# Optimization experiments

Hardware: AMD Instinct MI355X
Metric: run time of the kernel (lower is better)

## Reference

```python
import jax, jax.numpy as jnp
import numpy as np

NUM_HEADS = 32


def setup_inputs() -> dict:
    key = jax.random.key(0)
    ks = jax.random.split(key, 6)
    B, S, E = 1, 2048, 2560
    return {
        "hidden_states": jax.random.normal(ks[0], (B, S, E), dtype=jnp.float32),
        "attention_mask": jnp.zeros((B, 1, 1, S), dtype=jnp.float32),
        "position_bias": jax.random.normal(ks[1], (NUM_HEADS, S, S), dtype=jnp.float32),
        "c_attn_w": jax.random.normal(ks[2], (E, 3 * E), dtype=jnp.float32) * 0.02,
        "c_attn_b": jax.random.normal(ks[3], (3 * E,), dtype=jnp.float32) * 0.02,
        "c_proj_w": jax.random.normal(ks[4], (E, E), dtype=jnp.float32) * 0.02,
        "c_proj_b": jax.random.normal(ks[5], (E,), dtype=jnp.float32) * 0.02,
    }


def reference(hidden_states, attention_mask, position_bias, c_attn_w, c_attn_b, c_proj_w, c_proj_b):
    B, S, E = hidden_states.shape
    H = NUM_HEADS
    D = E // H  # head_dim = 80

    # Fused QKV projection (GPT2-style Conv1D: x @ W + b)
    qkv = hidden_states @ c_attn_w + c_attn_b            # [B, S, 3E]
    q, k, v = jnp.split(qkv, 3, axis=-1)

    def split_heads(t):
        return t.reshape(B, S, H, D).transpose(0, 2, 1, 3)  # [B, H, S, D]

    q, k, v = split_heads(q), split_heads(k), split_heads(v)

    # muP scaling: attn_scale_power=1.0 -> divide by head_dim (not sqrt)
    scores = jnp.einsum("bhqd,bhkd->bhqk", q, k) / jnp.asarray(D, q.dtype)
    scores = scores + attention_mask                     # additive mask [B,1,1,S]
    scores = scores + position_bias[None]                # ALiBi bias [1,H,S,S]

    attn = jax.nn.softmax(scores, axis=-1)               # dropout p=0 -> identity
    out = jnp.einsum("bhqk,bhkd->bhqd", attn, v)         # [B, H, S, D]
    out = out.transpose(0, 2, 1, 3).reshape(B, S, E)     # merge heads

    out = out @ c_proj_w + c_proj_b                      # output projection
    return out
```

## Files before the change

kernel.cpp:

```cpp
#include <hip/hip_runtime.h>
#include <stdint.h>

#define S_LEN 2048
#define EMB   2560
#define NH    32
#define HD    80
#define DP    96

typedef __bf16 bf16x8 __attribute__((ext_vector_type(8)));
typedef float  f32x4  __attribute__((ext_vector_type(4)));

__device__ __forceinline__ ushort f2bf(float x) {
    union { float f; uint32_t u; } v; v.f = x;
    return (ushort)((v.u + 0x7FFFu + ((v.u >> 16) & 1u)) >> 16);
}

__device__ __forceinline__ bf16x8 ldg8(const ushort* p) {
    return *reinterpret_cast<const bf16x8*>(p);
}

__device__ __forceinline__ void gload_lds16(const void* g, void* l) {
    __builtin_amdgcn_global_load_lds((__attribute__((address_space(1))) void*)g,
                                     (__attribute__((address_space(3))) void*)l,
                                     16, 0, 0);
}

__global__ void cvt_f32_bf16(const float* __restrict__ in, ushort* __restrict__ out, int n4) {
    int i = blockIdx.x * blockDim.x + threadIdx.x;
    if (i >= n4) return;
    float4 v = reinterpret_cast<const float4*>(in)[i];
    ushort4 r;
    r.x = f2bf(v.x); r.y = f2bf(v.y); r.z = f2bf(v.z); r.w = f2bf(v.w);
    reinterpret_cast<ushort4*>(out)[i] = r;
}

__global__ void transpose_cvt(const float* __restrict__ in, ushort* __restrict__ out, int R, int C) {
    __shared__ float tile[32][33];
    const int bx = blockIdx.x << 5;
    const int by = blockIdx.y << 5;
    const int tx = threadIdx.x, ty = threadIdx.y;
#pragma unroll
    for (int i = 0; i < 4; ++i)
        tile[ty + 8 * i][tx] = in[(size_t)(by + ty + 8 * i) * C + bx + tx];
    __syncthreads();
#pragma unroll
    for (int i = 0; i < 4; ++i)
        out[(size_t)(bx + ty + 8 * i) * R + by + tx] = f2bf(tile[tx][ty + 8 * i]);
}

__global__ void transpose_v(const ushort* __restrict__ V, ushort* __restrict__ VT) {
    __shared__ ushort tile[32][33];
    const int h  = blockIdx.z;
    const int bx = blockIdx.x << 5;
    const int by = blockIdx.y << 5;
    const int tx = threadIdx.x, ty = threadIdx.y;
    const ushort* vin  = V  + (size_t)h * S_LEN * HD;
    ushort*       vout = VT + (size_t)h * HD * S_LEN;
#pragma unroll
    for (int i = 0; i < 4; ++i) {
        int d = bx + tx, s = by + ty + 8 * i;
        tile[ty + 8 * i][tx] = (d < HD) ? vin[(size_t)s * HD + d] : (ushort)0;
    }
    __syncthreads();
#pragma unroll
    for (int i = 0; i < 4; ++i) {
        int d = bx + ty + 8 * i, s = by + tx;
        if (d < HD) vout[(size_t)d * S_LEN + s] = tile[tx][ty + 8 * i];
    }
}

template <int EPI>
__global__ __launch_bounds__(256)
void gemm_bt(const ushort* __restrict__ A, const ushort* __restrict__ BT,
             int M, int N, int Kd, const float* __restrict__ bvec,
             ushort* __restrict__ Qo, ushort* __restrict__ Ko, ushort* __restrict__ Vo,
             float* __restrict__ Co)
{
    __shared__ ushort As[128 * 64];
    __shared__ ushort Bs[128 * 64];

    const int nbn = N >> 7;
    const int nwg = gridDim.x;
    const int cpx = nwg >> 3;
    const int bid = blockIdx.x;
    const int wg  = (bid & 7) * cpx + (bid >> 3);
    const int bm  = wg / nbn;
    const int bn  = wg - bm * nbn;

    const int tid  = threadIdx.x;
    const int w    = tid >> 6, lane = tid & 63;
    const int lo   = lane & 15, hi = lane >> 4;
    const int wr   = w >> 1, wc = w & 1;

    const int srow  = tid >> 3;
    const int sbyte = (tid & 7) << 4;

    f32x4 acc[4][4] = {};

    const char* aG = (const char*)(A  + (size_t)bm * 128 * Kd);
    const char* bG = (const char*)(BT + (size_t)bn * 128 * Kd);
    const size_t rowBytes = (size_t)Kd * 2;

    for (int k0 = 0; k0 < Kd; k0 += 64) {
        __syncthreads();
#pragma unroll
        for (int is = 0; is < 4; ++is) {
            int r  = (is << 5) + srow;
            int sw = sbyte ^ ((r & 7) << 4);
            const char* ga = aG + (size_t)r * rowBytes + (size_t)k0 * 2 + sw;
            const char* gb = bG + (size_t)r * rowBytes + (size_t)k0 * 2 + sw;
            char* la = (char*)As + (is << 12) + (w << 10);
            char* lb = (char*)Bs + (is << 12) + (w << 10);
            gload_lds16(ga, la);
            gload_lds16(gb, lb);
        }
        asm volatile("s_waitcnt vmcnt(0)" ::: "memory");
        __syncthreads();
#pragma unroll
        for (int kk = 0; kk < 2; ++kk) {
            bf16x8 af[4], bf[4];
#pragma unroll
            for (int m = 0; m < 4; ++m) {
                int r   = (wr << 6) + (m << 4) + lo;
                int off = (r << 7) + ((((kk << 6) + (hi << 4))) ^ ((r & 7) << 4));
                af[m] = *(const bf16x8*)((const char*)As + off);
            }
#pragma unroll
            for (int n = 0; n < 4; ++n) {
                int r   = (wc << 6) + (n << 4) + lo;
                int off = (r << 7) + ((((kk << 6) + (hi << 4))) ^ ((r & 7) << 4));
                bf[n] = *(const bf16x8*)((const char*)Bs + off);
            }
#pragma unroll
            for (int m = 0; m < 4; ++m)
#pragma unroll
                for (int n = 0; n < 4; ++n)
                    acc[m][n] = __builtin_amdgcn_mfma_f32_16x16x32_bf16(af[m], bf[n], acc[m][n], 0, 0, 0);
        }
    }

    const int gr_base = bm * 128 + (wr << 6);
    const int gc_base = bn * 128 + (wc << 6);
#pragma unroll
    for (int m = 0; m < 4; ++m) {
        int gr0 = gr_base + (m << 4) + (hi << 2);
#pragma unroll
        for (int n = 0; n < 4; ++n) {
            int gc = gc_base + (n << 4) + lo;
            float bv = bvec[gc];
            if (EPI == 0) {
                int sec = gc / EMB;
                int rr  = gc - sec * EMB;
                int h   = rr / HD;
                int d   = rr - h * HD;
#pragma unroll
                for (int j = 0; j < 4; ++j) {
                    float vv = acc[m][n][j] + bv;
                    int s = gr0 + j;
                    if (sec == 0)      Qo[((size_t)h * S_LEN + s) * DP + d] = f2bf(vv * (1.0f / 80.0f));
                    else if (sec == 1) Ko[((size_t)h * S_LEN + s) * DP + d] = f2bf(vv);
                    else               Vo[((size_t)h * S_LEN + s) * HD + d] = f2bf(vv);
                }
            } else {
#pragma unroll
                for (int j = 0; j < 4; ++j)
                    Co[(size_t)(gr0 + j) * N + gc] = acc[m][n][j] + bv;
            }
        }
    }
}

__global__ __launch_bounds__(512, 4)
void attn_fwd(const ushort* __restrict__ Q, const ushort* __restrict__ K,
              const ushort* __restrict__ VT, const float* __restrict__ bias,
              const float* __restrict__ mask, ushort* __restrict__ ctx)
{
    __shared__ ushort Ks[2][64 * 96];
    __shared__ ushort Vs[2][80 * 64];
    __shared__ ushort P[8][16][72];

    const int bid = blockIdx.x;
    const int l_  = (bid & 7) * 64 + (bid >> 3);
    const int h   = l_ >> 4;
    const int qb  = (l_ & 15) << 7;
    const int tid = threadIdx.x;
    const int w   = tid >> 6, lane = tid & 63;
    const int lo  = lane & 15, hi = lane >> 4;
    const int qrow = qb + (w << 4);

    const ushort* qp = Q + ((size_t)(h * S_LEN + qrow + lo)) * DP + hi * 8;
    bf16x8 qf0 = ldg8(qp), qf1 = ldg8(qp + 32), qf2 = ldg8(qp + 64);

    const char*  kg = (const char*)(K + (size_t)h * S_LEN * DP);
    const char*  vg = (const char*)(VT + (size_t)h * HD * S_LEN);
    const float* bb = bias + (size_t)(h * S_LEN + qrow + hi * 4) * S_LEN + lo;

    f32x4 o[5] = {};
    float l_p[4] = {0.f, 0.f, 0.f, 0.f};
    float m_r[4] = {-1e30f, -1e30f, -1e30f, -1e30f};
    float bc[4][4], bn[4][4], mn_[4];

    auto stage_k = [&](int buf, int kt) {
        const char* src = kg + (size_t)kt * 192;
        gload_lds16(src + (w << 10) + lane * 16, (char*)Ks[buf] + (w << 10));
        if (w < 4)
            gload_lds16(src + ((w + 8) << 10) + lane * 16, (char*)Ks[buf] + ((w + 8) << 10));
    };
    auto stage_v = [&](int buf, int kt) {
        int r0 = (w << 3) + (lane >> 3);
        int s0 = ((lane & 7) << 4) ^ ((r0 & 7) << 4);
        gload_lds16(vg + (size_t)r0 * (S_LEN * 2) + (size_t)kt * 2 + s0,
                    (char*)Vs[buf] + (w << 10));
        if (w < 2) {
            int r1 = ((w + 8) << 3) + (lane >> 3);
            int s1 = ((lane & 7) << 4) ^ ((r1 & 7) << 4);
            gload_lds16(vg + (size_t)r1 * (S_LEN * 2) + (size_t)kt * 2 + s1,
                        (char*)Vs[buf] + ((w + 8) << 10));
        }
    };
    auto bload = [&](int kt) {
#pragma unroll
        for (int n = 0; n < 4; ++n) {
            mn_[n] = mask[kt + n * 16 + lo];
#pragma unroll
            for (int j = 0; j < 4; ++j)
                bn[n][j] = __builtin_nontemporal_load(bb + (size_t)j * S_LEN + kt + n * 16);
        }
    };
    auto rotate = [&]() {
#pragma unroll
        for (int n = 0; n < 4; ++n)
#pragma unroll
            for (int j = 0; j < 4; ++j)
                bc[n][j] = bn[n][j] + mn_[n];
    };

    stage_k(0, 0); stage_v(0, 0); bload(0); rotate();
    __syncthreads();

#pragma unroll 1
    for (int t = 0; t < 32; ++t) {
        const int kt = t << 6;
        const int cb = t & 1;
        if (t < 31) { stage_k(cb ^ 1, kt + 64); stage_v(cb ^ 1, kt + 64); bload(kt + 64); }

        const char* tb = (const char*)Ks[cb];
        f32x4 sc[4] = {};
        __builtin_amdgcn_s_setprio(1);
#pragma unroll
        for (int n = 0; n < 4; ++n) {
            const char* rp = tb + ((n << 4) + lo) * 192;
            sc[n] = __builtin_amdgcn_mfma_f32_16x16x32_bf16(qf0, *(const bf16x8*)(rp + hi * 16),       sc[n], 0, 0, 0);
            sc[n] = __builtin_amdgcn_mfma_f32_16x16x32_bf16(qf1, *(const bf16x8*)(rp + 64 + hi * 16),  sc[n], 0, 0, 0);
            sc[n] = __builtin_amdgcn_mfma_f32_16x16x32_bf16(qf2, *(const bf16x8*)(rp + 128 + hi * 16), sc[n], 0, 0, 0);
        }
        __builtin_amdgcn_s_setprio(0);

#pragma unroll
        for (int n = 0; n < 4; ++n)
#pragma unroll
            for (int j = 0; j < 4; ++j)
                sc[n][j] += bc[n][j];

        float tm[4];
#pragma unroll
        for (int j = 0; j < 4; ++j)
            tm[j] = fmaxf(fmaxf(sc[0][j], sc[1][j]), fmaxf(sc[2][j], sc[3][j]));
#pragma unroll
        for (int off = 1; off <= 8; off <<= 1)
#pragma unroll
            for (int j = 0; j < 4; ++j)
                tm[j] = fmaxf(tm[j], __shfl_xor(tm[j], off, 64));

        float al[4];
#pragma unroll
        for (int j = 0; j < 4; ++j) {
            float mnew = fmaxf(m_r[j], tm[j]);
            al[j] = __builtin_amdgcn_exp2f((m_r[j] - mnew) * 1.44269504f);
            m_r[j] = mnew;
            l_p[j] *= al[j];
        }
#pragma unroll
        for (int dn = 0; dn < 5; ++dn)
#pragma unroll
            for (int j = 0; j < 4; ++j)
                o[dn][j] *= al[j];
#pragma unroll
        for (int n = 0; n < 4; ++n)
#pragma unroll
            for (int j = 0; j < 4; ++j) {
                float p = __builtin_amdgcn_exp2f((sc[n][j] - m_r[j]) * 1.44269504f);
                l_p[j] += p;
                P[w][hi * 4 + j][n * 16 + lo] = f2bf(p);
            }
        asm volatile("s_waitcnt lgkmcnt(0)" ::: "memory");
        __builtin_amdgcn_sched_barrier(0);
        bf16x8 pf0 = ldg8(&P[w][lo][hi * 8]);
        bf16x8 pf1 = ldg8(&P[w][lo][32 + hi * 8]);

        const char* vb_ = (const char*)Vs[cb];
        __builtin_amdgcn_s_setprio(1);
#pragma unroll
        for (int dn = 0; dn < 5; ++dn) {
            const int rv = (dn << 4) + lo;
            const char* vp = vb_ + (rv << 7);
            const int sv = (rv & 7) << 4;
            o[dn] = __builtin_amdgcn_mfma_f32_16x16x32_bf16(pf0, *(const bf16x8*)(vp + ((hi * 16) ^ sv)),      o[dn], 0, 0, 0);
            o[dn] = __builtin_amdgcn_mfma_f32_16x16x32_bf16(pf1, *(const bf16x8*)(vp + ((64 + hi * 16) ^ sv)), o[dn], 0, 0, 0);
        }
        __builtin_amdgcn_s_setprio(0);

        rotate();
        __syncthreads();
    }

    float inv[4];
#pragma unroll
    for (int j = 0; j < 4; ++j) {
        float t = l_p[j];
        t += __shfl_xor(t, 1, 64); t += __shfl_xor(t, 2, 64);
        t += __shfl_xor(t, 4, 64); t += __shfl_xor(t, 8, 64);
        inv[j] = 1.0f / t;
    }
    ushort* cp = ctx + (size_t)(qrow + hi * 4) * EMB + h * HD + lo;
#pragma unroll
    for (int dn = 0; dn < 5; ++dn)
#pragma unroll
        for (int j = 0; j < 4; ++j)
            cp[(size_t)j * EMB + dn * 16] = f2bf(o[dn][j] * inv[j]);
}

extern "C" void kernel_launch(void* const* d_in, const int* in_sizes, int n_in,
                              void* d_out, int out_size, void* d_ws, size_t ws_size,
                              hipStream_t stream)
{
    const float* hs     = (const float*)d_in[0];
    const float* mask   = (const float*)d_in[1];
    const float* pbias  = (const float*)d_in[2];
    const float* attn_w = (const float*)d_in[3];
    const float* attn_b = (const float*)d_in[4];
    const float* proj_w = (const float*)d_in[5];
    const float* proj_b = (const float*)d_in[6];
    float* outp = (float*)d_out;

    char* ws = (char*)d_ws;
    ushort* hsB    = (ushort*)(ws);
    ushort* attnWT = (ushort*)(ws + 10485760ull);
    ushort* Qb     = (ushort*)(ws + 49807360ull);
    ushort* Kb     = (ushort*)(ws + 62390272ull);
    ushort* Vb     = (ushort*)(ws + 74973184ull);
    ushort* ctx    = hsB;
    ushort* VTb    = attnWT;
    ushort* projWT = attnWT;

    cvt_f32_bf16<<<5120, 256, 0, stream>>>(hs, hsB, 1310720);
    transpose_cvt<<<dim3(7680 / 32, 2560 / 32), dim3(32, 8), 0, stream>>>(attn_w, attnWT, 2560, 7680);
    hipMemsetAsync(Qb, 0, 12582912ull, stream);
    hipMemsetAsync(Kb, 0, 12582912ull, stream);

    gemm_bt<0><<<960, 256, 0, stream>>>(hsB, attnWT, 2048, 7680, 2560, attn_b,
                                        Qb, Kb, Vb, nullptr);

    transpose_v<<<dim3(3, 64, 32), dim3(32, 8), 0, stream>>>(Vb, VTb);

    attn_fwd<<<512, 512, 0, stream>>>(Qb, Kb, VTb, pbias, mask, ctx);

    transpose_cvt<<<dim3(2560 / 32, 2560 / 32), dim3(32, 8), 0, stream>>>(proj_w, projWT, 2560, 2560);

    gemm_bt<1><<<320, 256, 0, stream>>>(ctx, projWT, 2048, 2560, 2560, proj_b,
                                        nullptr, nullptr, nullptr, outp);
}
```

Before: 375.5 us.

## Write V transposed from QKV GEMM, zero only padding, swizzle K LDS

The QKV GEMM epilogue now stores V directly in head-transposed layout with packed 4-element writes, which removes the separate transpose_v kernel and its round trip through memory. The two full-buffer memsets of Q and K become a small kernel that zeroes only the padding columns 80-95. K tiles are loaded into LDS through an XOR-swizzled source offset and read back with the matching swizzle, to cut LDS bank conflicts in the QK^T MFMA reads. The swizzle on the last 64 bytes of each row uses a narrower mask, which must match between store and load for correctness.

```diff
diff --git a/kernel.cpp b/kernel.cpp
--- a/kernel.cpp
+++ b/kernel.cpp
@@ -34,6 +34,15 @@
     reinterpret_cast<ushort4*>(out)[i] = r;
 }
 
+__global__ void pad_zero(ushort* __restrict__ Qb, ushort* __restrict__ Kb) {
+    int i   = blockIdx.x * blockDim.x + threadIdx.x;
+    int row = i & 65535;
+    ushort* base = ((i >> 16) ? Kb : Qb) + (size_t)row * DP + HD;
+    uint4 z = {0, 0, 0, 0};
+    *reinterpret_cast<uint4*>(base)     = z;
+    *reinterpret_cast<uint4*>(base + 8) = z;
+}
+
 __global__ void transpose_cvt(const float* __restrict__ in, ushort* __restrict__ out, int R, int C) {
     __shared__ float tile[32][33];
     const int bx = blockIdx.x << 5;
@@ -46,27 +55,6 @@
 #pragma unroll
     for (int i = 0; i < 4; ++i)
         out[(size_t)(bx + ty + 8 * i) * R + by + tx] = f2bf(tile[tx][ty + 8 * i]);
-}
-
-__global__ void transpose_v(const ushort* __restrict__ V, ushort* __restrict__ VT) {
-    __shared__ ushort tile[32][33];
-    const int h  = blockIdx.z;
-    const int bx = blockIdx.x << 5;
-    const int by = blockIdx.y << 5;
-    const int tx = threadIdx.x, ty = threadIdx.y;
-    const ushort* vin  = V  + (size_t)h * S_LEN * HD;
-    ushort*       vout = VT + (size_t)h * HD * S_LEN;
-#pragma unroll
-    for (int i = 0; i < 4; ++i) {
-        int d = bx + tx, s = by + ty + 8 * i;
-        tile[ty + 8 * i][tx] = (d < HD) ? vin[(size_t)s * HD + d] : (ushort)0;
-    }
-    __syncthreads();
-#pragma unroll
-    for (int i = 0; i < 4; ++i) {
-        int d = bx + ty + 8 * i, s = by + tx;
-        if (d < HD) vout[(size_t)d * S_LEN + s] = tile[tx][ty + 8 * i];
-    }
 }
 
 template <int EPI>
@@ -153,13 +141,21 @@
                 int rr  = gc - sec * EMB;
                 int h   = rr / HD;
                 int d   = rr - h * HD;
-#pragma unroll
-                for (int j = 0; j < 4; ++j) {
-                    float vv = acc[m][n][j] + bv;
-                    int s = gr0 + j;
-                    if (sec == 0)      Qo[((size_t)h * S_LEN + s) * DP + d] = f2bf(vv * (1.0f / 80.0f));
-                    else if (sec == 1) Ko[((size_t)h * S_LEN + s) * DP + d] = f2bf(vv);
-                    else               Vo[((size_t)h * S_LEN + s) * HD + d] = f2bf(vv);
+                if (sec == 2) {
+                    ushort4 pk;
+                    pk.x = f2bf(acc[m][n][0] + bv);
+                    pk.y = f2bf(acc[m][n][1] + bv);
+                    pk.z = f2bf(acc[m][n][2] + bv);
+                    pk.w = f2bf(acc[m][n][3] + bv);
+                    *reinterpret_cast<ushort4*>(Vo + ((size_t)h * HD + d) * S_LEN + gr0) = pk;
+                } else {
+#pragma unroll
+                    for (int j = 0; j < 4; ++j) {
+                        float vv = acc[m][n][j] + bv;
+                        int s = gr0 + j;
+                        if (sec == 0) Qo[((size_t)h * S_LEN + s) * DP + d] = f2bf(vv * (1.0f / 80.0f));
+                        else          Ko[((size_t)h * S_LEN + s) * DP + d] = f2bf(vv);
+                    }
                 }
             } else {
 #pragma unroll
@@ -195,6 +191,16 @@
     const char*  vg = (const char*)(VT + (size_t)h * HD * S_LEN);
     const float* bb = bias + (size_t)(h * S_LEN + qrow + hi * 4) * S_LEN + lo;
 
+    int offK0, offK1;
+    {
+        int b0 = (w << 10) + lane * 16;
+        int r0 = b0 / 192, y0 = b0 - r0 * 192;
+        offK0 = r0 * 192 + (y0 ^ ((y0 < 128 ? (r0 & 7) : (r0 & 3)) << 4));
+        int b1 = ((w + 8) << 10) + lane * 16;
+        int r1 = b1 / 192, y1 = b1 - r1 * 192;
+        offK1 = r1 * 192 + (y1 ^ ((y1 < 128 ? (r1 & 7) : (r1 & 3)) << 4));
+    }
+
     f32x4 o[5] = {};
     float l_p[4] = {0.f, 0.f, 0.f, 0.f};
     float m_r[4] = {-1e30f, -1e30f, -1e30f, -1e30f};
@@ -202,9 +208,9 @@
 
     auto stage_k = [&](int buf, int kt) {
         const char* src = kg + (size_t)kt * 192;
-        gload_lds16(src + (w << 10) + lane * 16, (char*)Ks[buf] + (w << 10));
+        gload_lds16(src + offK0, (char*)Ks[buf] + (w << 10));
         if (w < 4)
-            gload_lds16(src + ((w + 8) << 10) + lane * 16, (char*)Ks[buf] + ((w + 8) << 10));
+            gload_lds16(src + offK1, (char*)Ks[buf] + ((w + 8) << 10));
     };
     auto stage_v = [&](int buf, int kt) {
         int r0 = (w << 3) + (lane >> 3);
@@ -249,10 +255,12 @@
         __builtin_amdgcn_s_setprio(1);
 #pragma unroll
         for (int n = 0; n < 4; ++n) {
-            const char* rp = tb + ((n << 4) + lo) * 192;
-            sc[n] = __builtin_amdgcn_mfma_f32_16x16x32_bf16(qf0, *(const bf16x8*)(rp + hi * 16),       sc[n], 0, 0, 0);
-            sc[n] = __builtin_amdgcn_mfma_f32_16x16x32_bf16(qf1, *(const bf16x8*)(rp + 64 + hi * 16),  sc[n], 0, 0, 0);
-            sc[n] = __builtin_amdgcn_mfma_f32_16x16x32_bf16(qf2, *(const bf16x8*)(rp + 128 + hi * 16), sc[n], 0, 0, 0);
+            const int r  = (n << 4) + lo;
+            const char* rp = tb + r * 192;
+            const int s7 = (r & 7) << 4, s3 = (r & 3) << 4;
+            sc[n] = __builtin_amdgcn_mfma_f32_16x16x32_bf16(qf0, *(const bf16x8*)(rp + ((hi * 16) ^ s7)),        sc[n], 0, 0, 0);
+            sc[n] = __builtin_amdgcn_mfma_f32_16x16x32_bf16(qf1, *(const bf16x8*)(rp + ((64 + hi * 16) ^ s7)),   sc[n], 0, 0, 0);
+            sc[n] = __builtin_amdgcn_mfma_f32_16x16x32_bf16(qf2, *(const bf16x8*)(rp + ((128 + hi * 16) ^ s3)),  sc[n], 0, 0, 0);
         }
         __builtin_amdgcn_s_setprio(0);
 
@@ -348,20 +356,16 @@
     ushort* attnWT = (ushort*)(ws + 10485760ull);
     ushort* Qb     = (ushort*)(ws + 49807360ull);
     ushort* Kb     = (ushort*)(ws + 62390272ull);
-    ushort* Vb     = (ushort*)(ws + 74973184ull);
+    ushort* VTb    = (ushort*)(ws + 74973184ull);
     ushort* ctx    = hsB;
-    ushort* VTb    = attnWT;
     ushort* projWT = attnWT;
 
     cvt_f32_bf16<<<5120, 256, 0, stream>>>(hs, hsB, 1310720);
     transpose_cvt<<<dim3(7680 / 32, 2560 / 32), dim3(32, 8), 0, stream>>>(attn_w, attnWT, 2560, 7680);
-    hipMemsetAsync(Qb, 0, 12582912ull, stream);
-    hipMemsetAsync(Kb, 0, 12582912ull, stream);
+    pad_zero<<<512, 256, 0, stream>>>(Qb, Kb);
 
     gemm_bt<0><<<960, 256, 0, stream>>>(hsB, attnWT, 2048, 7680, 2560, attn_b,
-                                        Qb, Kb, Vb, nullptr);
-
-    transpose_v<<<dim3(3, 64, 32), dim3(32, 8), 0, stream>>>(Vb, VTb);
+                                        Qb, Kb, VTb, nullptr);
 
     attn_fwd<<<512, 512, 0, stream>>>(Qb, Kb, VTb, pbias, mask, ctx);
 
```

Measured after the change: 371.2 us. Within noise of the previous version (-1.2%).
